# Kernel tuning notes

Hardware: AMD Instinct MI355X
Metric: run time of the kernel (lower is better)

Reference implementation:

```python
import jax, jax.numpy as jnp
import numpy as np

B, CIN, COUT, N, TIN = 8, 64, 64, 207, 54
K, NHID, SL, KT = 8, 64, 3, 3
HEADS, STRIDE, PL = 8, 4, 8
TIME_NUM, OUT_LEN = 120, 48
E = COUT * PL            # 512 = attention embed dim (embed_size*patch_len)
PD = E // HEADS          # 64 per-head dim
PNUM = (OUT_LEN + STRIDE - PL) // STRIDE + 1   # 12 patches
EPS = 1e-5


def setup_inputs():
    keys = iter(jax.random.split(jax.random.key(0), 48))
    def rn(shape, s):
        return jax.random.normal(next(keys), shape, jnp.float32) * s
    d = {}
    d['x'] = rn((B, CIN, N, TIN), 1.0)
    d['adj'] = jax.random.uniform(next(keys), (SL, N, N), jnp.float32) / N
    d['W_conv1'] = rn((COUT, CIN), 0.125); d['b_conv1'] = rn((COUT,), 0.02)
    d['g_T'] = jnp.ones((TIN,), jnp.float32); d['b_T'] = jnp.zeros((TIN,), jnp.float32)
    d['g_S'] = jnp.ones((N,), jnp.float32); d['b_S'] = jnp.zeros((N,), jnp.float32)
    d['W_time'] = rn((2*COUT, 3*COUT, 1, KT), 1.0/np.sqrt(3*COUT*KT)); d['b_time'] = rn((2*COUT,), 0.02)
    d['wq1'] = rn((SL, K, COUT, NHID), 0.125); d['wv1'] = rn((SL, K, COUT, NHID), 0.125)
    d['bias1'] = rn((SL, NHID), 0.05)
    d['wq2'] = rn((SL, K, NHID, 2*COUT), 0.125); d['wv2'] = rn((SL, K, NHID, 2*COUT), 0.125)
    d['bias2'] = rn((SL, 2*COUT), 0.05)
    d['W_mlp'] = rn((2*COUT, SL*2*COUT, 1, KT), 1.0/np.sqrt(SL*2*COUT*KT)); d['b_mlp'] = rn((2*COUT,), 0.02)
    d['emb_T'] = rn((TIME_NUM, E), 0.02)
    d['Wq'] = rn((PD, PD), 0.125); d['bq'] = rn((PD,), 0.02)
    d['Wk'] = rn((PD, PD), 0.125); d['bk'] = rn((PD,), 0.02)
    d['Wv'] = rn((PD, PD), 0.125); d['bv'] = rn((PD,), 0.02)
    d['W_fc'] = rn((E, E), 1.0/np.sqrt(E)); d['b_fc'] = rn((E,), 0.02)
    d['g1'] = jnp.ones((E,), jnp.float32); d['b1n'] = jnp.zeros((E,), jnp.float32)
    d['g2'] = jnp.ones((E,), jnp.float32); d['b2n'] = jnp.zeros((E,), jnp.float32)
    d['W_ff1'] = rn((E, 4*COUT), 1.0/np.sqrt(E)); d['b_ff1'] = rn((4*COUT,), 0.02)
    d['W_ff2'] = rn((4*COUT, E), 1.0/np.sqrt(4*COUT)); d['b_ff2'] = rn((E,), 0.02)
    d['W_rp'] = rn((PNUM*PL, OUT_LEN), 1.0/np.sqrt(PNUM*PL)); d['b_rp'] = rn((OUT_LEN,), 0.02)
    d['g_bn'] = jnp.ones((COUT,), jnp.float32); d['b_bn'] = jnp.zeros((COUT,), jnp.float32)
    return d


def _ln(v, g, b, axis):
    m = jnp.mean(v, axis=axis, keepdims=True)
    var = jnp.var(v, axis=axis, keepdims=True)
    xhat = (v - m) * jax.lax.rsqrt(var + EPS)
    shp = [1] * v.ndim; shp[axis] = -1
    return xhat * g.reshape(shp) + b.reshape(shp)


def _gconv(x, wq, wv, bias, a):
    # x: [B,C,N,L]; wq/wv: [K,C,D]; a: [N,N]  -- multi-basis sigmoid-gated GCN
    q = jnp.einsum('bcnl,kcd->kbdnl', x, wq)
    v = jnp.einsum('bcnl,kcd->kbdnl', x, wv)
    s = jnp.sum(jax.nn.sigmoid(q) * v, axis=0)           # [B,D,N,L]
    out = jnp.einsum('nk,bcnl->bckl', a, s)              # adjacency aggregation (exact index order of source)
    return out + bias[None, :, None, None]


def _conv2d(x, w, b, dil):
    y = jax.lax.conv_general_dilated(x, w, (1, 1), 'VALID', rhs_dilation=(1, dil),
                                     dimension_numbers=('NCHW', 'OIHW', 'NCHW'))
    return y + b[None, :, None, None]


def reference(x, adj, W_conv1, b_conv1, g_T, b_T, g_S, b_S, W_time, b_time,
              wq1, wv1, bias1, wq2, wv2, bias2, W_mlp, b_mlp, emb_T,
              Wq, bq, Wk, bk, Wv, bv, W_fc, b_fc, g1, b1n, g2, b2n,
              W_ff1, b_ff1, W_ff2, b_ff2, W_rp, b_rp, g_bn, b_bn):
    residual = jnp.einsum('oc,bcnl->bonl', W_conv1, x) + b_conv1[None, :, None, None]
    xcat = jnp.concatenate([residual, _ln(residual, g_T, b_T, 3), _ln(residual, g_S, b_S, 2)], axis=1)
    h = _conv2d(xcat, W_time, b_time, 2)                 # [B,2C,N,50]
    h = jnp.tanh(h[:, :COUT]) * jax.nn.sigmoid(h[:, COUT:])
    outs = [_gconv(jax.nn.relu(_gconv(h, wq1[i], wv1[i], bias1[i], adj[i])),
                   wq2[i], wv2[i], bias2[i], adj[i]) for i in range(SL)]
    g = _conv2d(jnp.concatenate(outs, axis=1), W_mlp, b_mlp, 1)   # [B,2C,N,48]
    g = jnp.tanh(g[:, :COUT]) * jax.nn.sigmoid(g[:, COUT:])      # [B,C,N,48]
    # --- TTransformer with patching ---
    z = jnp.pad(g, ((0, 0), (0, 0), (0, 0), (0, STRIDE)))        # pad time by stride (52 >= patch_len)
    idx = jnp.arange(PNUM)[:, None] * STRIDE + jnp.arange(PL)[None, :]
    patches = z[..., idx]                                        # [B,C,N,P,PL] unfold
    q0 = patches.reshape(B, N, PNUM, E)                          # row-major reshape, as in torch source
    xe = q0 + emb_T[:PNUM][None, None]
    qh = xe.reshape(B, N, PNUM, HEADS, PD)
    qs = qh @ Wq + bq; ks = qh @ Wk + bk; vs = qh @ Wv + bv
    scores = jnp.einsum('bnqhd,bnkhd->bnqkh', qs, ks)
    att = jax.nn.softmax(scores / jnp.sqrt(jnp.float32(E)), axis=2)   # softmax over QUERY axis (faithful to source)
    ao = jnp.einsum('bnqkh,bnkhd->bnqhd', att, vs).reshape(B, N, PNUM, E) @ W_fc + b_fc
    M = _ln(ao + xe, g1, b1n, 3)
    ff = jax.nn.relu(M @ W_ff1 + b_ff1) @ W_ff2 + b_ff2
    U = _ln(M + ff, g2, b2n, 3)
    o = (U + xe + M).reshape(B, N, COUT, PNUM * PL) @ W_rp + b_rp     # [B,N,C,48]
    o = jnp.transpose(o, (0, 2, 1, 3))                               # [B,C,N,48]
    # --- BatchNorm2d (training-mode batch stats) over residual sum ---
    y = o + residual[..., -OUT_LEN:]
    m = jnp.mean(y, axis=(0, 2, 3), keepdims=True)
    var = jnp.var(y, axis=(0, 2, 3), keepdims=True)
    return (y - m) * jax.lax.rsqrt(var + EPS) * g_bn[None, :, None, None] + b_bn[None, :, None, None]
```

## Files before the change

kernel.cpp:

```cpp
#include <hip/hip_runtime.h>
#include <hip/hip_bf16.h>

#define TPB 256
#define TPA 512

constexpr int Bx = 8, Cc = 64, Nn = 207, Tin = 54, Kb = 8;
constexpr int LP = 52, NP = Nn * LP;
constexpr int NPa = 10816;
constexpr int L50 = 50, Tout = 48;
constexpr int Ee = 512, Pn = 12;
constexpr float EPSF = 1e-5f;
constexpr int SRDF = 516;

constexpr size_t O_RESID = 0;
constexpr size_t O_LNTM  = O_RESID + (size_t)Bx*Cc*Nn*Tin;
constexpr size_t O_LNTR  = O_LNTM  + (size_t)Bx*Cc*Nn;
constexpr size_t O_LNSM  = O_LNTR  + (size_t)Bx*Cc*Nn;
constexpr size_t O_LNSR  = O_LNSM  + (size_t)Bx*Cc*Tin;
constexpr size_t O_XCAT  = O_LNSR  + (size_t)Bx*Cc*Tin;
constexpr size_t O_RB    = O_XCAT  + (size_t)Bx*192*Nn*Tin;
constexpr size_t O_H     = O_RB    + (size_t)Bx*128*NP;
constexpr size_t O_GACC  = O_H     + (size_t)Bx*64*NP;
constexpr size_t O_GG    = O_GACC  + (size_t)Bx*128*Nn*Tout;
constexpr size_t O_XE    = O_GG    + (size_t)Bx*64*Nn*Tout;
constexpr size_t O_WTT   = O_XE    + (size_t)Bx*Nn*Pn*Ee;
constexpr size_t O_WTM   = O_WTT   + (size_t)128*192*3;
constexpr size_t O_BNST  = O_WTM   + (size_t)128*384*3;
constexpr size_t O_WTB   = O_BNST + 128;
constexpr size_t O_ADJT  = O_WTB  + (size_t)128*576/2;
constexpr size_t O_HT    = O_H;
constexpr size_t O_TAIL  = O_XCAT + (size_t)Bx*128*NP;
constexpr size_t O_WQ1B  = O_TAIL + (size_t)Bx*NPa*64/2;
constexpr size_t O_WV1B  = O_WQ1B + (size_t)24*64*64/2;
constexpr size_t O_WQ2B  = O_WV1B + (size_t)24*64*64/2;
constexpr size_t O_WV2B  = O_WQ2B + (size_t)24*128*64/2;
constexpr size_t O_RBT   = O_WV2B + (size_t)24*128*64/2;
constexpr size_t O_WQT   = O_RBT  + (size_t)Bx*NPa*64/2;
constexpr size_t O_WKT   = O_WQT  + 2048;
constexpr size_t O_WVT   = O_WKT  + 2048;
constexpr size_t O_WFCT  = O_WVT  + 2048;
constexpr size_t O_WF1T  = O_WFCT + 131072;
constexpr size_t O_WF2T  = O_WF1T + 65536;

#define FMA4(acc, sA_, vB_) { (acc).x += (sA_)*(vB_).x; (acc).y += (sA_)*(vB_).y; (acc).z += (sA_)*(vB_).z; (acc).w += (sA_)*(vB_).w; }

typedef __attribute__((ext_vector_type(8))) short bf16x8;
typedef __attribute__((ext_vector_type(4))) float f32x4;

__device__ __forceinline__ float sigm(float x){ return 1.0f/(1.0f+__expf(-x)); }
__device__ __forceinline__ ushort f2bf(float x){ __hip_bfloat16 h = __float2bfloat16(x); return *(ushort*)&h; }

__global__ __launch_bounds__(TPB) void k_residual(const float* __restrict__ x, const float* __restrict__ W,
                                                  const float* __restrict__ bias, float* __restrict__ out){
  int n = blockIdx.x, b = blockIdx.y;
  __shared__ __align__(16) float sX[Cc][Tin];
  __shared__ __align__(16) float sW[Cc*Cc];
  int tid = threadIdx.x;
  for(int i=tid;i<Cc*Tin;i+=TPB){ int c=i/Tin, l=i%Tin; sX[c][l] = x[((size_t)(b*Cc+c)*Nn+n)*Tin+l]; }
  for(int i=tid;i<Cc*Cc;i+=TPB) sW[i]=W[i];
  __syncthreads();
  for(int i=tid;i<Cc*Tin;i+=TPB){
    int o=i/Tin, l=i%Tin; float acc=bias[o];
    #pragma unroll 8
    for(int c=0;c<Cc;c++) acc += sW[o*Cc+c]*sX[c][l];
    out[((size_t)(b*Cc+o)*Nn+n)*Tin+l]=acc;
  }
}

__global__ __launch_bounds__(TPB) void k_lnT(const float* __restrict__ r, float* __restrict__ mean, float* __restrict__ rstd){
  int row = blockIdx.x*TPB + threadIdx.x;
  if(row >= Bx*Cc*Nn) return;
  const float* p = r + (size_t)row*Tin;
  float s=0.f,s2=0.f;
  for(int l=0;l<Tin;l++){ float v=p[l]; s+=v; s2+=v*v; }
  float m=s*(1.f/Tin); float var=s2*(1.f/Tin)-m*m;
  mean[row]=m; rstd[row]=rsqrtf(fmaxf(var,0.f)+EPSF);
}
__global__ __launch_bounds__(TPB) void k_lnS(const float* __restrict__ r, float* __restrict__ mean, float* __restrict__ rstd){
  int row = blockIdx.x*TPB + threadIdx.x;
  if(row >= Bx*Cc*Tin) return;
  int l = row % Tin; int bc = row / Tin;
  const float* p = r + (size_t)bc*Nn*Tin + l;
  float s=0.f,s2=0.f;
  for(int n=0;n<Nn;n++){ float v=p[(size_t)n*Tin]; s+=v; s2+=v*v; }
  float m=s*(1.f/Nn); float var=s2*(1.f/Nn)-m*m;
  mean[row]=m; rstd[row]=rsqrtf(fmaxf(var,0.f)+EPSF);
}

struct WJob { const float* W; ushort* F; int K, N, KS, NT, sStride, total; };
struct WJobs { WJob j[11]; };

__global__ __launch_bounds__(TPB) void k_wfrag_all(WJobs jobs){
  int gi = blockIdx.x*TPB + threadIdx.x;
  for(int seg=0; seg<11; seg++){
    const WJob J = jobs.j[seg];
    if(gi < J.total){
      int i = gi;
      int j = i & 7; int lane = (i>>3) & 63;
      int t = i >> 9;
      int ks = t % J.KS; int r = t / J.KS; int colTile = r % J.NT; int s = r / J.NT;
      int r15 = lane & 15, hi = lane >> 4;
      int k = ks*32 + hi*8 + j, col = colTile*16 + r15;
      float v = (k < J.K && col < J.N) ? J.W[(size_t)s*J.sStride + (size_t)k*J.N + col] : 0.f;
      J.F[i] = f2bf(v);
      return;
    }
    gi -= J.total;
  }
}

__global__ __launch_bounds__(TPB) void k_wtbF(const float* __restrict__ W, ushort* __restrict__ F){
  int i = blockIdx.x*TPB + threadIdx.x;
  if(i >= 8*18*512) return;
  int j = i & 7; int lane = (i>>3) & 63;
  int t = i >> 9;
  int ks = t % 18; int colTile = t / 18;
  int r15 = lane & 15, hi = lane >> 4;
  int k = ks*32 + hi*8 + j, o = colTile*16 + r15;
  int kt = k/192, ci = k - kt*192;
  F[i] = f2bf(W[(size_t)(o*192+ci)*3 + kt]);
}

__global__ __launch_bounds__(TPB) void k_wmlpF(const float* __restrict__ W, ushort* __restrict__ F){
  int i = blockIdx.x*TPB + threadIdx.x;
  if(i >= 3*8*12*512) return;
  int j = i & 7; int lane = (i>>3) & 63;
  int t = i >> 9;
  int ks = t % 12; int r = t / 12; int colTile = r & 7; int layer = r >> 3;
  int r15 = lane & 15, hi = lane >> 4;
  int k = ks*32 + hi*8 + j;
  int kt = k >> 7, ci = k & 127;
  int o = colTile*16 + r15;
  F[i] = f2bf(W[(size_t)(o*384 + layer*128 + ci)*3 + kt]);
}

template<int C>
__global__ __launch_bounds__(TPB) void k_t2bf(const float* __restrict__ X, ushort* __restrict__ XT){
  int p0 = blockIdx.x*64, b = blockIdx.y;
  int tid = threadIdx.x;
  __shared__ __align__(16) float sT[64][65];
  for(int cc=0; cc<C; cc+=64){
    if(cc) __syncthreads();
    for(int i=tid;i<4096;i+=TPB){ int c=i>>6, col=i&63; int p=p0+col;
      sT[c][col] = (p<NP) ? X[((size_t)(b*C+cc+c))*NP + p] : 0.f; }
    __syncthreads();
    for(int i=tid;i<512;i+=TPB){
      int row=i>>3, c8=(i&7)<<3;
      ushort u[8];
      #pragma unroll
      for(int j=0;j<8;j++) u[j] = f2bf(sT[c8+j][row]);
      *(uint4*)&XT[((size_t)b*NPa + p0 + row)*C + cc + c8] = *(uint4*)u;
    }
  }
}

__global__ __launch_bounds__(TPB) void k_timeconv_mfma(const float* __restrict__ resid,
    const float* __restrict__ tm, const float* __restrict__ tr,
    const float* __restrict__ sm, const float* __restrict__ sr,
    const float* __restrict__ gT, const float* __restrict__ bT,
    const float* __restrict__ gS, const float* __restrict__ bS,
    const ushort* __restrict__ WF, const float* __restrict__ bias, ushort* __restrict__ HT){
  int n = blockIdx.x, b = blockIdx.y;
  constexpr int XS = 200;
  __shared__ __align__(16) ushort sXT[68*XS];
  int tid = threadIdx.x;
  for(int i=tid; i<14*XS; i+=TPB) sXT[54*XS + i] = 0;
  float gSn = gS[n], bSn = bS[n];
  for(int i=tid; i<64*54; i+=TPB){
    int cm = i/54, l = i%54;
    int rowT = (b*Cc+cm)*Nn + n;
    float r = resid[(size_t)rowT*Tin + l];
    float v1 = (r - tm[rowT]) * tr[rowT] * gT[l] + bT[l];
    int rowS = (b*Cc+cm)*Tin + l;
    float v2 = (r - sm[rowS]) * sr[rowS] * gSn + bSn;
    sXT[l*XS + cm]        = f2bf(r);
    sXT[l*XS + 64 + cm]   = f2bf(v1);
    sXT[l*XS + 128 + cm]  = f2bf(v2);
  }
  __syncthreads();
  int lane = tid & 63, w = tid >> 6;
  int r15 = lane & 15, hi = lane >> 4;
  float b0 = bias[w*16 + r15], b1 = bias[w*16 + 64 + r15];
  f32x4 acc0[4], acc1[4];
  #pragma unroll
  for(int tt=0;tt<4;tt++){
    acc0[tt][0]=b0; acc0[tt][1]=b0; acc0[tt][2]=b0; acc0[tt][3]=b0;
    acc1[tt][0]=b1; acc1[tt][1]=b1; acc1[tt][2]=b1; acc1[tt][3]=b1;
  }
  const ushort* wp0 = WF + ((size_t)w*18)*512 + lane*8;
  const ushort* wp1 = WF + ((size_t)(w+4)*18)*512 + lane*8;
  #pragma unroll 2
  for(int ks=0; ks<18; ks++){
    int k0 = ks*32 + hi*8;
    int kt = k0/192, ci0 = k0 - kt*192;
    bf16x8 bw0 = *(const bf16x8*)&wp0[(size_t)ks*512];
    bf16x8 bw1 = *(const bf16x8*)&wp1[(size_t)ks*512];
    #pragma unroll
    for(int tt=0;tt<4;tt++){
      bf16x8 ax = *(const bf16x8*)&sXT[(tt*16 + r15 + 2*kt)*XS + ci0];
      acc0[tt] = __builtin_amdgcn_mfma_f32_16x16x32_bf16(ax, bw0, acc0[tt], 0,0,0);
      acc1[tt] = __builtin_amdgcn_mfma_f32_16x16x32_bf16(ax, bw1, acc1[tt], 0,0,0);
    }
  }
  ushort* htp = HT + ((size_t)b*NPa + (size_t)n*LP)*64;
  int c = w*16 + r15;
  #pragma unroll
  for(int tt=0;tt<4;tt++){
    int t0 = tt*16 + hi*4;
    #pragma unroll
    for(int i=0;i<4;i++){
      int t = t0 + i;
      if(t < L50) htp[(size_t)t*64 + c] = f2bf(tanhf(acc0[tt][i])*sigm(acc1[tt][i]));
    }
  }
  if(tid < 128){ int cz = tid >> 1, tz = 50 + (tid & 1); htp[(size_t)tz*64 + cz] = 0; }
}

__global__ __launch_bounds__(TPB) void k_htpad(ushort* __restrict__ HT){
  int i = blockIdx.x*TPB + threadIdx.x;
  int per = (NPa-NP)*8;
  if(i >= Bx*per) return;
  int b = i / per, r = i % per;
  uint4 z; z.x=0;z.y=0;z.z=0;z.w=0;
  *(uint4*)&HT[((size_t)b*NPa + NP)*64 + (size_t)r*8] = z;
}

template<int D>
__global__ __launch_bounds__(TPB) void k_gcs_mfma(const ushort* __restrict__ XT,
    const ushort* __restrict__ wqF, const ushort* __restrict__ wvF,
    float* __restrict__ S){
  constexpr int Dt = D/16;
  int p0 = blockIdx.x*64;
  int b = blockIdx.z;
  int tid = threadIdx.x;
  int lane = tid & 63, w = tid >> 6;
  int d0 = blockIdx.y*64 + (w<<4);
  int dTile = blockIdx.y*4 + w;
  __shared__ __align__(16) ushort sX[64*64];
  for(int i=tid;i<512;i+=TPB){
    int row=i>>3, c8=(i&7)<<3;
    uint4 v = *(const uint4*)&XT[((size_t)b*NPa + p0 + row)*64 + c8];
    *(uint4*)&sX[row*64 + (c8 ^ ((row&7)<<3))] = v;
  }
  __syncthreads();
  int r15 = lane & 15, hi = lane >> 4;
  bf16x8 bf[4][2];
  #pragma unroll
  for(int pt=0;pt<4;pt++){
    int row = pt*16 + r15;
    int sw = (row&7)<<3;
    int cu0 = hi*8;
    bf[pt][0] = *(const bf16x8*)&sX[row*64 + (cu0 ^ sw)];
    bf[pt][1] = *(const bf16x8*)&sX[row*64 + ((cu0+32) ^ sw)];
  }
  f32x4 acc[4];
  #pragma unroll
  for(int pt=0;pt<4;pt++){ acc[pt][0]=0.f; acc[pt][1]=0.f; acc[pt][2]=0.f; acc[pt][3]=0.f; }
  const ushort* wqp = wqF + ((size_t)dTile*2)*512 + lane*8;
  const ushort* wvp = wvF + ((size_t)dTile*2)*512 + lane*8;
  for(int k=0;k<Kb;k++){
    bf16x8 aq0 = *(const bf16x8*)&wqp[0];
    bf16x8 aq1 = *(const bf16x8*)&wqp[512];
    bf16x8 av0 = *(const bf16x8*)&wvp[0];
    bf16x8 av1 = *(const bf16x8*)&wvp[512];
    wqp += (size_t)Dt*2*512; wvp += (size_t)Dt*2*512;
    #pragma unroll
    for(int pt=0;pt<4;pt++){
      f32x4 q; q[0]=0.f;q[1]=0.f;q[2]=0.f;q[3]=0.f;
      f32x4 v; v[0]=0.f;v[1]=0.f;v[2]=0.f;v[3]=0.f;
      q = __builtin_amdgcn_mfma_f32_16x16x32_bf16(aq0, bf[pt][0], q, 0,0,0);
      q = __builtin_amdgcn_mfma_f32_16x16x32_bf16(aq1, bf[pt][1], q, 0,0,0);
      v = __builtin_amdgcn_mfma_f32_16x16x32_bf16(av0, bf[pt][0], v, 0,0,0);
      v = __builtin_amdgcn_mfma_f32_16x16x32_bf16(av1, bf[pt][1], v, 0,0,0);
      #pragma unroll
      for(int i=0;i<4;i++) acc[pt][i] += v[i]*sigm(q[i]);
    }
  }
  #pragma unroll
  for(int pt=0;pt<4;pt++){
    int p = p0 + pt*16 + r15;
    if(p < NP){
      #pragma unroll
      for(int i=0;i<4;i++){
        int d = d0 + hi*4 + i;
        S[((size_t)b*D + d)*NP + p] = acc[pt][i];
      }
    }
  }
}

template<int RELU>
__global__ __launch_bounds__(TPB) void k_agg_mfma(const float* __restrict__ S, const ushort* __restrict__ adjF,
                                                  const float* __restrict__ bias, float* __restrict__ Out, int D){
  int d = blockIdx.x, b = blockIdx.y;
  int bd = b*D + d;
  constexpr int SST = 232;
  __shared__ __align__(16) ushort sB[64*SST];
  int tid = threadIdx.x;
  for(int i=tid*8; i<64*SST; i+=TPB*8){ uint4 z; z.x=0;z.y=0;z.z=0;z.w=0; *(uint4*)&sB[i]=z; }
  __syncthreads();
  const float* Sp = S + (size_t)bd*NP;
  for(int i=tid; i<NP; i+=TPB){
    int nn = i/52, l = i - nn*52;
    sB[l*SST + nn] = f2bf(Sp[i]);
  }
  __syncthreads();
  int lane = tid & 63, w = tid >> 6;
  int r15 = lane & 15, hi = lane >> 4;
  float bb = bias[d];
  float* Op = Out + (size_t)bd*NP;
  for(int k2t = w; k2t < 13; k2t += 4){
    f32x4 acc[4];
    #pragma unroll
    for(int lt=0;lt<4;lt++){ acc[lt][0]=0;acc[lt][1]=0;acc[lt][2]=0;acc[lt][3]=0; }
    #pragma unroll
    for(int ks=0; ks<7; ks++){
      bf16x8 a = *(const bf16x8*)&adjF[((size_t)(k2t*7 + ks))*512 + lane*8];
      #pragma unroll
      for(int lt=0;lt<4;lt++){
        bf16x8 bfr = *(const bf16x8*)&sB[(lt*16+r15)*SST + ks*32 + hi*8];
        acc[lt] = __builtin_amdgcn_mfma_f32_16x16x32_bf16(a, bfr, acc[lt], 0,0,0);
      }
    }
    #pragma unroll
    for(int lt=0;lt<4;lt++){
      #pragma unroll
      for(int i2=0;i2<4;i2++){
        int k2 = k2t*16 + hi*4 + i2;
        int l  = lt*16 + r15;
        if(k2 < Nn && l < LP){
          float v = acc[lt][i2] + bb;
          if(RELU) v = fmaxf(v, 0.f);
          Op[(size_t)k2*LP + l] = v;
        }
      }
    }
  }
}

template<int MODE>
__global__ __launch_bounds__(TPB) void k_mlpacc_mfma(const float* __restrict__ RB, const ushort* __restrict__ WF,
                                                     float* __restrict__ gacc, const float* __restrict__ bm,
                                                     float* __restrict__ gg){
  int n = blockIdx.x, b = blockIdx.y;
  constexpr int CS = 136;
  __shared__ __align__(16) ushort sLT[52*CS];
  int tid = threadIdx.x;
  for(int i=tid;i<6656;i+=TPB){
    int c = i/52, l = i%52;
    sLT[l*CS + c] = f2bf(RB[(((size_t)b*128+c)*Nn + n)*LP + l]);
  }
  __syncthreads();
  int lane = tid & 63, w = tid >> 6;
  int r15 = lane & 15, hi = lane >> 4;
  f32x4 acc0[3], acc1[3];
  #pragma unroll
  for(int tt=0;tt<3;tt++){
    acc0[tt][0]=0;acc0[tt][1]=0;acc0[tt][2]=0;acc0[tt][3]=0;
    acc1[tt][0]=0;acc1[tt][1]=0;acc1[tt][2]=0;acc1[tt][3]=0;
  }
  const ushort* wp0 = WF + ((size_t)w*12)*512 + lane*8;
  const ushort* wp1 = WF + ((size_t)(w+4)*12)*512 + lane*8;
  #pragma unroll 3
  for(int ks=0; ks<12; ks++){
    int kt = ks>>2, ci0 = (ks&3)*32 + hi*8;
    bf16x8 bw0 = *(const bf16x8*)&wp0[(size_t)ks*512];
    bf16x8 bw1 = *(const bf16x8*)&wp1[(size_t)ks*512];
    #pragma unroll
    for(int tt=0;tt<3;tt++){
      bf16x8 ax = *(const bf16x8*)&sLT[(tt*16 + r15 + kt)*CS + ci0];
      acc0[tt] = __builtin_amdgcn_mfma_f32_16x16x32_bf16(ax, bw0, acc0[tt], 0,0,0);
      acc1[tt] = __builtin_amdgcn_mfma_f32_16x16x32_bf16(ax, bw1, acc1[tt], 0,0,0);
    }
  }
  int o = w*16 + r15;
  if(MODE < 2){
    float* gp = gacc + ((size_t)b*Nn + n)*48*128;
    #pragma unroll
    for(int tt=0;tt<3;tt++){
      #pragma unroll
      for(int i2=0;i2<4;i2++){
        int tq = tt*16 + hi*4 + i2;
        size_t a0 = (size_t)tq*128 + o;
        if(MODE==0){ gp[a0] = acc0[tt][i2]; gp[a0+64] = acc1[tt][i2]; }
        else       { gp[a0] += acc0[tt][i2]; gp[a0+64] += acc1[tt][i2]; }
      }
    }
  } else {
    const float* gp = gacc + ((size_t)b*Nn + n)*48*128;
    float b0 = bm[o], b1 = bm[o+64];
    float* ggp = gg + (((size_t)b*Cc + o)*Nn + n)*(size_t)Tout;
    #pragma unroll
    for(int tt=0;tt<3;tt++){
      #pragma unroll
      for(int i2=0;i2<4;i2++){
        int tq = tt*16 + hi*4 + i2;
        size_t a0 = (size_t)tq*128 + o;
        float a  = gp[a0]    + acc0[tt][i2] + b0;
        float g2 = gp[a0+64] + acc1[tt][i2] + b1;
        ggp[tq] = tanhf(a)*sigm(g2);
      }
    }
  }
}

__global__ __launch_bounds__(TPB) void k_xe(const float* __restrict__ gg, const float* __restrict__ emb, float* __restrict__ xe){
  size_t i = (size_t)blockIdx.x*TPB + threadIdx.x;
  if(i >= (size_t)Bx*1271808) return;
  int b = (int)(i / 1271808);
  int off = (int)(i % 1271808);
  int c = off / 19872; int r = off % 19872;
  int n = r / 96; int r2 = r % 96;
  int p = r2 >> 3; int j = r2 & 7;
  int t = p*4 + j;
  float v = 0.f;
  if(t < Tout) v = gg[(((size_t)b*Cc+c)*Nn + n)*Tout + t];
  int e = off & 511; int p2 = (off >> 9) % 12;
  xe[i] = v + emb[(size_t)p2*Ee + e];
}

template<int NW>
__device__ __forceinline__ void ln_rows(float* buf, const float* __restrict__ g, const float* __restrict__ be, int tid){
  int lane = tid & 63, wv = tid >> 6;
  for(int r = wv; r < 12; r += NW){
    float s=0.f, s2=0.f;
    #pragma unroll
    for(int j=0;j<8;j++){ float v = buf[r*SRDF + j*64 + lane]; s+=v; s2+=v*v; }
    #pragma unroll
    for(int off=32; off; off>>=1){ s += __shfl_xor(s,off); s2 += __shfl_xor(s2,off); }
    float m = s*(1.f/512.f);
    float rstd = rsqrtf(fmaxf(s2*(1.f/512.f)-m*m, 0.f)+EPSF);
    #pragma unroll
    for(int j=0;j<8;j++){ int e = j*64+lane; float v = buf[r*SRDF+e];
      buf[r*SRDF+e] = (v-m)*rstd*g[e] + be[e]; }
  }
}

__global__ __launch_bounds__(TPA,2) void k_attn(
    const float* __restrict__ xe, const float* __restrict__ resid,
    const ushort* __restrict__ WqF, const float* __restrict__ bq,
    const ushort* __restrict__ WkF, const float* __restrict__ bk,
    const ushort* __restrict__ WvF, const float* __restrict__ bv,
    const ushort* __restrict__ WfcF, const float* __restrict__ bfc,
    const float* __restrict__ g1, const float* __restrict__ b1n,
    const float* __restrict__ g2, const float* __restrict__ b2n,
    const ushort* __restrict__ Wff1F, const float* __restrict__ bff1,
    const ushort* __restrict__ Wff2F, const float* __restrict__ bff2,
    const float* __restrict__ Wrp, const float* __restrict__ brp,
    float* __restrict__ y)
{
  int n = blockIdx.x, b = blockIdx.y;
  __shared__ __align__(16) ushort SbX[16*512];
  __shared__ __align__(16) ushort Mb[16*256];
  __shared__ __align__(16) float U0[12*SRDF];
  __shared__ __align__(16) float U1[12*SRDF];
  __shared__ __align__(16) float sS[1160];
  int tid = threadIdx.x;
  int lane = tid & 63, w = tid >> 6;
  int r15 = lane & 15, hi = lane >> 4;
  const float* __restrict__ xeg = xe + ((size_t)b*Nn + n)*6144;

  for(int i=tid;i<1024;i+=TPA){
    int r = i>>6, ch = i&63;
    ushort u[8];
    if(r<12){
      const float* s = &xeg[r*512 + ch*8];
      #pragma unroll
      for(int j=0;j<8;j++) u[j] = f2bf(s[j]);
    } else {
      #pragma unroll
      for(int j=0;j<8;j++) u[j] = 0;
    }
    *(uint4*)&SbX[r*512 + ((ch ^ (r&7))<<3)] = *(uint4*)u;
  }
  for(int i=tid;i<128;i+=TPA){
    int r = 12 + (i>>5), ch = i&31;
    uint4 z; z.x=0;z.y=0;z.z=0;z.w=0;
    *(uint4*)&Mb[r*256 + ch*8] = z;
  }
  __syncthreads();

  f32x4 vfrag[4];
  {
    int head = w;
    bf16x8 a0, a1;
    { int ch0 = head*8 + hi, ch1 = head*8 + 4 + hi;
      a0 = *(const bf16x8*)&SbX[r15*512 + ((ch0 ^ (r15&7))<<3)];
      a1 = *(const bf16x8*)&SbX[r15*512 + ((ch1 ^ (r15&7))<<3)]; }
    #pragma unroll
    for(int nt=0;nt<4;nt++){
      int col = nt*16 + r15;
      float bb = bq[col];
      f32x4 acc; acc[0]=bb;acc[1]=bb;acc[2]=bb;acc[3]=bb;
      acc = __builtin_amdgcn_mfma_f32_16x16x32_bf16(a0, *(const bf16x8*)&WqF[(size_t)(nt*2+0)*512 + lane*8], acc, 0,0,0);
      acc = __builtin_amdgcn_mfma_f32_16x16x32_bf16(a1, *(const bf16x8*)&WqF[(size_t)(nt*2+1)*512 + lane*8], acc, 0,0,0);
      #pragma unroll
      for(int i2=0;i2<4;i2++){ int p = hi*4+i2; if(p<12) U0[p*SRDF + head*64 + col] = acc[i2]; }
    }
    #pragma unroll
    for(int nt=0;nt<4;nt++){
      int col = nt*16 + r15;
      float bb = bk[col];
      f32x4 acc; acc[0]=bb;acc[1]=bb;acc[2]=bb;acc[3]=bb;
      acc = __builtin_amdgcn_mfma_f32_16x16x32_bf16(a0, *(const bf16x8*)&WkF[(size_t)(nt*2+0)*512 + lane*8], acc, 0,0,0);
      acc = __builtin_amdgcn_mfma_f32_16x16x32_bf16(a1, *(const bf16x8*)&WkF[(size_t)(nt*2+1)*512 + lane*8], acc, 0,0,0);
      #pragma unroll
      for(int i2=0;i2<4;i2++){ int p = hi*4+i2; if(p<12) U1[p*SRDF + head*64 + col] = acc[i2]; }
    }
    #pragma unroll
    for(int nt=0;nt<4;nt++){
      int col = nt*16 + r15;
      float bb = bv[col];
      f32x4 acc; acc[0]=bb;acc[1]=bb;acc[2]=bb;acc[3]=bb;
      acc = __builtin_amdgcn_mfma_f32_16x16x32_bf16(a0, *(const bf16x8*)&WvF[(size_t)(nt*2+0)*512 + lane*8], acc, 0,0,0);
      acc = __builtin_amdgcn_mfma_f32_16x16x32_bf16(a1, *(const bf16x8*)&WvF[(size_t)(nt*2+1)*512 + lane*8], acc, 0,0,0);
      vfrag[nt] = acc;
    }
  }
  __syncthreads();

  const float scale = 0.04419417382415922f;
  for(int i=tid;i<1152;i+=TPA){
    int q = i%12, kh = i/12; int h2 = kh&7, k2 = kh>>3;
    const float* qp = &U0[q*SRDF + h2*64];
    const float* kp = &U1[k2*SRDF + h2*64];
    float s=0.f;
    #pragma unroll
    for(int d4=0; d4<16; d4++){
      float4 a4 = *(const float4*)&qp[d4*4];
      float4 b4 = *(const float4*)&kp[d4*4];
      s += a4.x*b4.x + a4.y*b4.y + a4.z*b4.z + a4.w*b4.w;
    }
    sS[i] = s*scale;
  }
  __syncthreads();
  {
    int head = w;
    #pragma unroll
    for(int nt=0;nt<4;nt++){
      int col = nt*16 + r15;
      #pragma unroll
      for(int i2=0;i2<4;i2++){ int p = hi*4+i2; if(p<12) U0[p*SRDF + head*64 + col] = vfrag[nt][i2]; }
    }
  }
  if(tid<96){
    float mx=-1e30f;
    for(int q=0;q<12;q++) mx = fmaxf(mx, sS[tid*12+q]);
    float sm=0.f;
    for(int q=0;q<12;q++){ float e = __expf(sS[tid*12+q]-mx); sS[tid*12+q]=e; sm+=e; }
    float inv = 1.f/sm;
    for(int q=0;q<12;q++) sS[tid*12+q] *= inv;
  }
  __syncthreads();

  for(int i=tid;i<6144;i+=TPA){
    int q=i>>9, h2=(i>>6)&7, d=i&63;
    float s=0.f;
    #pragma unroll
    for(int k2=0;k2<12;k2++) s += sS[(k2*8+h2)*12+q]*U0[k2*SRDF+h2*64+d];
    int kk = i & 511;
    SbX[q*512 + (((kk>>3) ^ (q&7))<<3) + (kk&7)] = f2bf(s);
  }
  __syncthreads();

  {
    f32x4 acc[4];
    #pragma unroll
    for(int nt=0;nt<4;nt++){ float bb = bfc[(w*4+nt)*16 + r15]; acc[nt][0]=bb;acc[nt][1]=bb;acc[nt][2]=bb;acc[nt][3]=bb; }
    for(int ks=0;ks<16;ks++){
      int ch = ks*4 + hi;
      bf16x8 a = *(const bf16x8*)&SbX[r15*512 + ((ch ^ (r15&7))<<3)];
      #pragma unroll
      for(int nt=0;nt<4;nt++){
        acc[nt] = __builtin_amdgcn_mfma_f32_16x16x32_bf16(a, *(const bf16x8*)&WfcF[(size_t)((w*4+nt)*16 + ks)*512 + lane*8], acc[nt], 0,0,0);
      }
    }
    #pragma unroll
    for(int nt=0;nt<4;nt++){
      int col = (w*4+nt)*16 + r15;
      #pragma unroll
      for(int i2=0;i2<4;i2++){ int p = hi*4+i2; if(p<12) U1[p*SRDF + col] = acc[nt][i2] + xeg[p*512 + col]; }
    }
  }
  __syncthreads();
  ln_rows<8>(U1, g1, b1n, tid);
  __syncthreads();

  for(int i=tid;i<6144;i+=TPA){
    int r=i>>9, kk=i&511;
    SbX[r*512 + (((kk>>3) ^ (r&7))<<3) + (kk&7)] = f2bf(U1[r*SRDF + kk]);
  }
  __syncthreads();

  {
    f32x4 acc[2];
    #pragma unroll
    for(int nt=0;nt<2;nt++){ float bb = bff1[(w*2+nt)*16 + r15]; acc[nt][0]=bb;acc[nt][1]=bb;acc[nt][2]=bb;acc[nt][3]=bb; }
    for(int ks=0;ks<16;ks++){
      int ch = ks*4 + hi;
      bf16x8 a = *(const bf16x8*)&SbX[r15*512 + ((ch ^ (r15&7))<<3)];
      #pragma unroll
      for(int nt=0;nt<2;nt++){
        acc[nt] = __builtin_amdgcn_mfma_f32_16x16x32_bf16(a, *(const bf16x8*)&Wff1F[(size_t)((w*2+nt)*16 + ks)*512 + lane*8], acc[nt], 0,0,0);
      }
    }
    #pragma unroll
    for(int nt=0;nt<2;nt++){
      int u = (w*2+nt)*16 + r15;
      #pragma unroll
      for(int i2=0;i2<4;i2++){
        int p = hi*4+i2;
        if(p<12) Mb[p*256 + (((u>>3) ^ (p&7))<<3) + (u&7)] = f2bf(fmaxf(acc[nt][i2], 0.f));
      }
    }
  }
  __syncthreads();

  {
    f32x4 acc[4];
    #pragma unroll
    for(int nt=0;nt<4;nt++){ float bb = bff2[(w*4+nt)*16 + r15]; acc[nt][0]=bb;acc[nt][1]=bb;acc[nt][2]=bb;acc[nt][3]=bb; }
    for(int ks=0;ks<8;ks++){
      int ch = ks*4 + hi;
      bf16x8 a = *(const bf16x8*)&Mb[r15*256 + ((ch ^ (r15&7))<<3)];
      #pragma unroll
      for(int nt=0;nt<4;nt++){
        acc[nt] = __builtin_amdgcn_mfma_f32_16x16x32_bf16(a, *(const bf16x8*)&Wff2F[(size_t)((w*4+nt)*8 + ks)*512 + lane*8], acc[nt], 0,0,0);
      }
    }
    #pragma unroll
    for(int nt=0;nt<4;nt++){
      int col = (w*4+nt)*16 + r15;
      #pragma unroll
      for(int i2=0;i2<4;i2++){ int p = hi*4+i2; if(p<12) U0[p*SRDF + col] = acc[nt][i2] + U1[p*SRDF + col]; }
    }
  }
  __syncthreads();
  ln_rows<8>(U0, g2, b2n, tid);
  __syncthreads();

  for(int i=tid;i<6144;i+=TPA){
    int r=i>>9, c=i&511;
    U1[r*SRDF+c] = U0[r*SRDF+c] + U1[r*SRDF+c] + xeg[r*512+c];
  }
  __syncthreads();
  for(int i=tid;i<4608;i+=TPA) U0[i] = Wrp[i];
  __syncthreads();
  #pragma unroll
  for(int j=0;j<2;j++){
    int i4 = tid + j*TPA;
    if(i4 < 768){
      int c = i4/12, tq = i4%12; int t0 = tq*4;
      float4 acc = *(const float4*)&brp[t0];
      for(int t96=0;t96<96;t96++){
        int f = c*96 + t96;
        float a = U1[(f>>9)*SRDF + (f&511)];
        float4 w4 = *(const float4*)&U0[t96*48 + t0];
        FMA4(acc, a, w4);
      }
      size_t rb = (((size_t)b*Cc+c)*Nn + n)*Tin + 6 + t0;
      acc.x += resid[rb+0]; acc.y += resid[rb+1]; acc.z += resid[rb+2]; acc.w += resid[rb+3];
      *(float4*)&y[(((size_t)b*Cc+c)*Nn + n)*Tout + t0] = acc;
    }
  }
}

__global__ __launch_bounds__(TPB) void k_bnstats(const float* __restrict__ y, float* __restrict__ stats){
  int c = blockIdx.x; int tid = threadIdx.x;
  float s=0.f,s2=0.f;
  const int per = Nn*Tout;
  for(int idx=tid; idx<Bx*per; idx+=TPB){
    int b = idx/per, r = idx%per;
    float v = y[((size_t)b*Cc+c)*per + r];
    s+=v; s2+=v*v;
  }
  __shared__ float rs[TPB], rs2[TPB];
  rs[tid]=s; rs2[tid]=s2; __syncthreads();
  for(int off=TPB/2; off; off>>=1){ if(tid<off){ rs[tid]+=rs[tid+off]; rs2[tid]+=rs2[tid+off]; } __syncthreads(); }
  if(tid==0){
    float m = rs[0]/(float)(Bx*per);
    float var = rs2[0]/(float)(Bx*per) - m*m;
    stats[c]=m; stats[64+c]=rsqrtf(fmaxf(var,0.f)+EPSF);
  }
}
__global__ __launch_bounds__(TPB) void k_bnout(const float* __restrict__ y, const float* __restrict__ stats,
                                               const float* __restrict__ gbn, const float* __restrict__ bbn,
                                               float* __restrict__ out){
  size_t i = (size_t)blockIdx.x*TPB + threadIdx.x;
  if(i >= (size_t)Bx*Cc*Nn*Tout) return;
  int c = (int)((i/(Nn*Tout))%Cc);
  out[i] = (y[i]-stats[c])*stats[64+c]*gbn[c] + bbn[c];
}

extern "C" void kernel_launch(void* const* d_in, const int* in_sizes, int n_in,
                              void* d_out, int out_size, void* d_ws, size_t ws_size,
                              hipStream_t stream) {
  const float* x      = (const float*)d_in[0];
  const float* adj    = (const float*)d_in[1];
  const float* Wconv1 = (const float*)d_in[2];
  const float* bconv1 = (const float*)d_in[3];
  const float* gT     = (const float*)d_in[4];
  const float* bT     = (const float*)d_in[5];
  const float* gS     = (const float*)d_in[6];
  const float* bS     = (const float*)d_in[7];
  const float* Wtime  = (const float*)d_in[8];
  const float* btime  = (const float*)d_in[9];
  const float* wq1    = (const float*)d_in[10];
  const float* wv1    = (const float*)d_in[11];
  const float* bias1  = (const float*)d_in[12];
  const float* wq2    = (const float*)d_in[13];
  const float* wv2    = (const float*)d_in[14];
  const float* bias2  = (const float*)d_in[15];
  const float* Wmlp   = (const float*)d_in[16];
  const float* bmlp   = (const float*)d_in[17];
  const float* embT   = (const float*)d_in[18];
  const float* Wq     = (const float*)d_in[19];
  const float* bq     = (const float*)d_in[20];
  const float* Wk     = (const float*)d_in[21];
  const float* bk     = (const float*)d_in[22];
  const float* Wv     = (const float*)d_in[23];
  const float* bv     = (const float*)d_in[24];
  const float* Wfc    = (const float*)d_in[25];
  const float* bfc    = (const float*)d_in[26];
  const float* g1     = (const float*)d_in[27];
  const float* b1n    = (const float*)d_in[28];
  const float* g2     = (const float*)d_in[29];
  const float* b2n    = (const float*)d_in[30];
  const float* Wff1   = (const float*)d_in[31];
  const float* bff1   = (const float*)d_in[32];
  const float* Wff2   = (const float*)d_in[33];
  const float* bff2   = (const float*)d_in[34];
  const float* Wrp    = (const float*)d_in[35];
  const float* brp    = (const float*)d_in[36];
  const float* gbn    = (const float*)d_in[37];
  const float* bbn    = (const float*)d_in[38];

  float* ws = (float*)d_ws;
  float* RESID = ws + O_RESID;
  float* LNTM  = ws + O_LNTM;
  float* LNTR  = ws + O_LNTR;
  float* LNSM  = ws + O_LNSM;
  float* LNSR  = ws + O_LNSR;
  float* RA    = ws + O_XCAT;
  float* RB    = ws + O_RB;
  float* GACC  = ws + O_GACC;
  float* GG    = ws + O_GG;
  float* Y     = ws + O_GG;
  float* XE    = ws + O_XE;
  float* BNST  = ws + O_BNST;
  ushort* WTMF = (ushort*)(ws + O_WTM);
  ushort* WTB  = (ushort*)(ws + O_WTB);
  ushort* ADJT = (ushort*)(ws + O_ADJT);
  ushort* HT   = (ushort*)(ws + O_HT);
  ushort* WQ1B = (ushort*)(ws + O_WQ1B);
  ushort* WV1B = (ushort*)(ws + O_WV1B);
  ushort* WQ2B = (ushort*)(ws + O_WQ2B);
  ushort* WV2B = (ushort*)(ws + O_WV2B);
  ushort* RBT  = (ushort*)(ws + O_RBT);
  ushort* WQT  = (ushort*)(ws + O_WQT);
  ushort* WKT  = (ushort*)(ws + O_WKT);
  ushort* WVT  = (ushort*)(ws + O_WVT);
  ushort* WFCT = (ushort*)(ws + O_WFCT);
  ushort* WF1T = (ushort*)(ws + O_WF1T);
  ushort* WF2T = (ushort*)(ws + O_WF2T);

  k_residual<<<dim3(Nn,Bx),TPB,0,stream>>>(x, Wconv1, bconv1, RESID);
  k_lnT<<<(Bx*Cc*Nn)/TPB,TPB,0,stream>>>(RESID, LNTM, LNTR);
  k_lnS<<<(Bx*Cc*Tin)/TPB,TPB,0,stream>>>(RESID, LNSM, LNSR);
  k_wtbF<<<(8*18*512+TPB-1)/TPB,TPB,0,stream>>>(Wtime, WTB);
  k_wmlpF<<<(3*8*12*512+TPB-1)/TPB,TPB,0,stream>>>(Wmlp, WTMF);
  k_htpad<<<(Bx*(NPa-NP)*8+TPB-1)/TPB,TPB,0,stream>>>(HT);
  k_timeconv_mfma<<<dim3(Nn,Bx),TPB,0,stream>>>(RESID, LNTM, LNTR, LNSM, LNSR, gT, bT, gS, bS,
                                                WTB, btime, HT);

  WJobs jobs;
  jobs.j[0]  = { wq1,  WQ1B, 64,  64,  2,  4,  64*64,   24*4*2*512 };
  jobs.j[1]  = { wv1,  WV1B, 64,  64,  2,  4,  64*64,   24*4*2*512 };
  jobs.j[2]  = { wq2,  WQ2B, 64,  128, 2,  8,  64*128,  24*8*2*512 };
  jobs.j[3]  = { wv2,  WV2B, 64,  128, 2,  8,  64*128,  24*8*2*512 };
  jobs.j[4]  = { Wq,   WQT,  64,  64,  2,  4,  64*64,   4*2*512 };
  jobs.j[5]  = { Wk,   WKT,  64,  64,  2,  4,  64*64,   4*2*512 };
  jobs.j[6]  = { Wv,   WVT,  64,  64,  2,  4,  64*64,   4*2*512 };
  jobs.j[7]  = { Wfc,  WFCT, 512, 512, 16, 32, 512*512, 32*16*512 };
  jobs.j[8]  = { Wff1, WF1T, 512, 256, 16, 16, 512*256, 16*16*512 };
  jobs.j[9]  = { Wff2, WF2T, 256, 512, 8,  32, 256*512, 32*8*512 };
  jobs.j[10] = { adj,  ADJT, 207, 207, 7,  13, Nn*Nn,   3*13*7*512 };
  int totalW = 2*(24*4*2*512) + 2*(24*8*2*512) + 3*(4*2*512) + 32*16*512 + 16*16*512 + 32*8*512 + 3*13*7*512;
  k_wfrag_all<<<(totalW+TPB-1)/TPB,TPB,0,stream>>>(jobs);

  for(int i=0;i<3;i++){
    k_gcs_mfma<64><<<dim3(169,1,Bx),TPB,0,stream>>>(HT, WQ1B+(size_t)i*8*4*2*512, WV1B+(size_t)i*8*4*2*512, RA);
    k_agg_mfma<1><<<dim3(64,Bx),TPB,0,stream>>>(RA, ADJT+(size_t)i*13*7*512, bias1+(size_t)i*64, RB, 64);
    k_t2bf<64><<<dim3(169,Bx),TPB,0,stream>>>(RB, RBT);
    k_gcs_mfma<128><<<dim3(169,2,Bx),TPB,0,stream>>>(RBT, WQ2B+(size_t)i*8*8*2*512, WV2B+(size_t)i*8*8*2*512, RA);
    k_agg_mfma<0><<<dim3(128,Bx),TPB,0,stream>>>(RA, ADJT+(size_t)i*13*7*512, bias2+(size_t)i*128, RB, 128);
    if(i==0)      k_mlpacc_mfma<0><<<dim3(Nn,Bx),TPB,0,stream>>>(RB, WTMF+(size_t)i*8*12*512, GACC, bmlp, GG);
    else if(i==1) k_mlpacc_mfma<1><<<dim3(Nn,Bx),TPB,0,stream>>>(RB, WTMF+(size_t)i*8*12*512, GACC, bmlp, GG);
    else          k_mlpacc_mfma<2><<<dim3(Nn,Bx),TPB,0,stream>>>(RB, WTMF+(size_t)i*8*12*512, GACC, bmlp, GG);
  }
  k_xe<<<(Bx*1271808)/TPB,TPB,0,stream>>>(GG, embT, XE);
  k_attn<<<dim3(Nn,Bx),TPA,0,stream>>>(XE, RESID, WQT,bq, WKT,bk, WVT,bv, WFCT,bfc,
                                       g1,b1n,g2,b2n, WF1T,bff1, WF2T,bff2, Wrp,brp, Y);
  k_bnstats<<<64,TPB,0,stream>>>(Y, BNST);
  k_bnout<<<(Bx*Cc*Nn*Tout)/TPB,TPB,0,stream>>>(Y, BNST, gbn, bbn, (float*)d_out);
}
```

Baseline: 900.2 us.

## Fuse time-LayerNorm stats into residual conv and inline xe gather into attention

The time-axis LayerNorm statistics are now computed inside the residual 1x1 conv kernel from a shared-memory copy of its output, which removes the separate k_lnT launch and a re-read of the residual tensor. The materialised xe buffer (about 40 MB of writes and reads) is dropped, and k_attn recomputes each xe element on the fly from GG plus the embedding through a scattered index mapping. It does that at three separate points in the kernel. The trade-off is extra integer division and uncoalesced gather loads in k_attn, plus more shared memory in k_residual. The Y output buffer moves to the old XE slot so it no longer aliases GG, which k_attn still reads.

```diff
diff --git a/kernel.cpp b/kernel.cpp
--- a/kernel.cpp
+++ b/kernel.cpp
@@ -50,11 +50,23 @@
 __device__ __forceinline__ float sigm(float x){ return 1.0f/(1.0f+__expf(-x)); }
 __device__ __forceinline__ ushort f2bf(float x){ __hip_bfloat16 h = __float2bfloat16(x); return *(ushort*)&h; }
 
+__device__ __forceinline__ float xe_val(const float* __restrict__ gg, const float* __restrict__ emb,
+                                        int b, int n2, int p2, int e){
+  int flat = n2*6144 + p2*512 + e;
+  int c = flat / 19872; int rem = flat - c*19872;
+  int ns = rem / 96;    int r2  = rem - ns*96;
+  int t = (r2>>3)*4 + (r2&7);
+  float v = (t < Tout) ? gg[(((size_t)b*Cc + c)*Nn + ns)*(size_t)Tout + t] : 0.f;
+  return v + emb[(size_t)p2*Ee + e];
+}
+
 __global__ __launch_bounds__(TPB) void k_residual(const float* __restrict__ x, const float* __restrict__ W,
-                                                  const float* __restrict__ bias, float* __restrict__ out){
+                                                  const float* __restrict__ bias, float* __restrict__ out,
+                                                  float* __restrict__ lnm, float* __restrict__ lnr){
   int n = blockIdx.x, b = blockIdx.y;
   __shared__ __align__(16) float sX[Cc][Tin];
   __shared__ __align__(16) float sW[Cc*Cc];
+  __shared__ __align__(16) float sO[Cc][Tin];
   int tid = threadIdx.x;
   for(int i=tid;i<Cc*Tin;i+=TPB){ int c=i/Tin, l=i%Tin; sX[c][l] = x[((size_t)(b*Cc+c)*Nn+n)*Tin+l]; }
   for(int i=tid;i<Cc*Cc;i+=TPB) sW[i]=W[i];
@@ -64,18 +76,18 @@
     #pragma unroll 8
     for(int c=0;c<Cc;c++) acc += sW[o*Cc+c]*sX[c][l];
     out[((size_t)(b*Cc+o)*Nn+n)*Tin+l]=acc;
-  }
-}
-
-__global__ __launch_bounds__(TPB) void k_lnT(const float* __restrict__ r, float* __restrict__ mean, float* __restrict__ rstd){
-  int row = blockIdx.x*TPB + threadIdx.x;
-  if(row >= Bx*Cc*Nn) return;
-  const float* p = r + (size_t)row*Tin;
-  float s=0.f,s2=0.f;
-  for(int l=0;l<Tin;l++){ float v=p[l]; s+=v; s2+=v*v; }
-  float m=s*(1.f/Tin); float var=s2*(1.f/Tin)-m*m;
-  mean[row]=m; rstd[row]=rsqrtf(fmaxf(var,0.f)+EPSF);
-}
+    sO[o][l]=acc;
+  }
+  __syncthreads();
+  if(tid < Cc){
+    float s=0.f,s2=0.f;
+    for(int l=0;l<Tin;l++){ float v=sO[tid][l]; s+=v; s2+=v*v; }
+    float m=s*(1.f/Tin); float var=s2*(1.f/Tin)-m*m;
+    int row = (b*Cc+tid)*Nn + n;
+    lnm[row]=m; lnr[row]=rsqrtf(fmaxf(var,0.f)+EPSF);
+  }
+}
+
 __global__ __launch_bounds__(TPB) void k_lnS(const float* __restrict__ r, float* __restrict__ mean, float* __restrict__ rstd){
   int row = blockIdx.x*TPB + threadIdx.x;
   if(row >= Bx*Cc*Tin) return;
@@ -404,21 +416,6 @@
   }
 }
 
-__global__ __launch_bounds__(TPB) void k_xe(const float* __restrict__ gg, const float* __restrict__ emb, float* __restrict__ xe){
-  size_t i = (size_t)blockIdx.x*TPB + threadIdx.x;
-  if(i >= (size_t)Bx*1271808) return;
-  int b = (int)(i / 1271808);
-  int off = (int)(i % 1271808);
-  int c = off / 19872; int r = off % 19872;
-  int n = r / 96; int r2 = r % 96;
-  int p = r2 >> 3; int j = r2 & 7;
-  int t = p*4 + j;
-  float v = 0.f;
-  if(t < Tout) v = gg[(((size_t)b*Cc+c)*Nn + n)*Tout + t];
-  int e = off & 511; int p2 = (off >> 9) % 12;
-  xe[i] = v + emb[(size_t)p2*Ee + e];
-}
-
 template<int NW>
 __device__ __forceinline__ void ln_rows(float* buf, const float* __restrict__ g, const float* __restrict__ be, int tid){
   int lane = tid & 63, wv = tid >> 6;
@@ -437,7 +434,7 @@
 }
 
 __global__ __launch_bounds__(TPA,2) void k_attn(
-    const float* __restrict__ xe, const float* __restrict__ resid,
+    const float* __restrict__ gg, const float* __restrict__ emb, const float* __restrict__ resid,
     const ushort* __restrict__ WqF, const float* __restrict__ bq,
     const ushort* __restrict__ WkF, const float* __restrict__ bk,
     const ushort* __restrict__ WvF, const float* __restrict__ bv,
@@ -458,15 +455,13 @@
   int tid = threadIdx.x;
   int lane = tid & 63, w = tid >> 6;
   int r15 = lane & 15, hi = lane >> 4;
-  const float* __restrict__ xeg = xe + ((size_t)b*Nn + n)*6144;
 
   for(int i=tid;i<1024;i+=TPA){
     int r = i>>6, ch = i&63;
     ushort u[8];
     if(r<12){
-      const float* s = &xeg[r*512 + ch*8];
-      #pragma unroll
-      for(int j=0;j<8;j++) u[j] = f2bf(s[j]);
+      #pragma unroll
+      for(int j=0;j<8;j++) u[j] = f2bf(xe_val(gg, emb, b, n, r, ch*8 + j));
     } else {
       #pragma unroll
       for(int j=0;j<8;j++) u[j] = 0;
@@ -579,7 +574,7 @@
     for(int nt=0;nt<4;nt++){
       int col = (w*4+nt)*16 + r15;
       #pragma unroll
-      for(int i2=0;i2<4;i2++){ int p = hi*4+i2; if(p<12) U1[p*SRDF + col] = acc[nt][i2] + xeg[p*512 + col]; }
+      for(int i2=0;i2<4;i2++){ int p = hi*4+i2; if(p<12) U1[p*SRDF + col] = acc[nt][i2] + xe_val(gg, emb, b, n, p, col); }
     }
   }
   __syncthreads();
@@ -641,7 +636,7 @@
 
   for(int i=tid;i<6144;i+=TPA){
     int r=i>>9, c=i&511;
-    U1[r*SRDF+c] = U0[r*SRDF+c] + U1[r*SRDF+c] + xeg[r*512+c];
+    U1[r*SRDF+c] = U0[r*SRDF+c] + U1[r*SRDF+c] + xe_val(gg, emb, b, n, r, c);
   }
   __syncthreads();
   for(int i=tid;i<4608;i+=TPA) U0[i] = Wrp[i];
@@ -745,8 +740,7 @@
   float* RB    = ws + O_RB;
   float* GACC  = ws + O_GACC;
   float* GG    = ws + O_GG;
-  float* Y     = ws + O_GG;
-  float* XE    = ws + O_XE;
+  float* Y     = ws + O_XE;
   float* BNST  = ws + O_BNST;
   ushort* WTMF = (ushort*)(ws + O_WTM);
   ushort* WTB  = (ushort*)(ws + O_WTB);
@@ -764,8 +758,7 @@
   ushort* WF1T = (ushort*)(ws + O_WF1T);
   ushort* WF2T = (ushort*)(ws + O_WF2T);
 
-  k_residual<<<dim3(Nn,Bx),TPB,0,stream>>>(x, Wconv1, bconv1, RESID);
-  k_lnT<<<(Bx*Cc*Nn)/TPB,TPB,0,stream>>>(RESID, LNTM, LNTR);
+  k_residual<<<dim3(Nn,Bx),TPB,0,stream>>>(x, Wconv1, bconv1, RESID, LNTM, LNTR);
   k_lnS<<<(Bx*Cc*Tin)/TPB,TPB,0,stream>>>(RESID, LNSM, LNSR);
   k_wtbF<<<(8*18*512+TPB-1)/TPB,TPB,0,stream>>>(Wtime, WTB);
   k_wmlpF<<<(3*8*12*512+TPB-1)/TPB,TPB,0,stream>>>(Wmlp, WTMF);
@@ -798,8 +791,7 @@
     else if(i==1) k_mlpacc_mfma<1><<<dim3(Nn,Bx),TPB,0,stream>>>(RB, WTMF+(size_t)i*8*12*512, GACC, bmlp, GG);
     else          k_mlpacc_mfma<2><<<dim3(Nn,Bx),TPB,0,stream>>>(RB, WTMF+(size_t)i*8*12*512, GACC, bmlp, GG);
   }
-  k_xe<<<(Bx*1271808)/TPB,TPB,0,stream>>>(GG, embT, XE);
-  k_attn<<<dim3(Nn,Bx),TPA,0,stream>>>(XE, RESID, WQT,bq, WKT,bk, WVT,bv, WFCT,bfc,
+  k_attn<<<dim3(Nn,Bx),TPA,0,stream>>>(GG, embT, RESID, WQT,bq, WKT,bk, WVT,bv, WFCT,bfc,
                                        g1,b1n,g2,b2n, WF1T,bff1, WF2T,bff2, Wrp,brp, Y);
   k_bnstats<<<64,TPB,0,stream>>>(Y, BNST);
   k_bnout<<<(Bx*Cc*Nn*Tout)/TPB,TPB,0,stream>>>(Y, BNST, gbn, bbn, (float*)d_out);
```

New measurement: 909.7 us. About the same (+1.1%).
